# Optimization experiments

Hardware: AMD Instinct MI355X
Metric: run time of the kernel (lower is better)

Reference implementation:

```python
import jax, jax.numpy as jnp
import numpy as np

N = 20000
E = 320000
NEG_SLOPE = 0.2
BN_EPS = 1e-5


def _segment_softmax(e, dst, n):
    # e: [E, H] attention logits, dst: [E] destination node ids
    m = jax.ops.segment_max(e, dst, num_segments=n)           # [N, H]
    ex = jnp.exp(e - m[dst])                                   # [E, H]
    s = jax.ops.segment_sum(ex, dst, num_segments=n)          # [N, H]
    return ex / s[dst]


def gat_conv(x, src, dst, W, a_src, a_dst, b, heads, out_ch):
    # PyG GATConv (concat=True): h = x @ W reshaped to [N, H, C]
    n = x.shape[0]
    h = (x @ W).reshape(n, heads, out_ch)                      # [N, H, C]
    al_s = jnp.einsum('nhc,hc->nh', h, a_src)                  # [N, H]
    al_d = jnp.einsum('nhc,hc->nh', h, a_dst)
    e = jax.nn.leaky_relu(al_s[src] + al_d[dst], NEG_SLOPE)    # [E, H]
    alpha = _segment_softmax(e, dst, n)                        # [E, H]
    msg = h[src] * alpha[:, :, None]                           # [E, H, C]
    out = jax.ops.segment_sum(msg, dst, num_segments=n)        # [N, H, C]
    return out.reshape(n, heads * out_ch) + b


def batch_norm(x, gamma, beta):
    mu = jnp.mean(x, axis=0)
    var = jnp.mean((x - mu) ** 2, axis=0)  # biased, as torch BN training
    return gamma * (x - mu) * jax.lax.rsqrt(var + BN_EPS) + beta


def setup_inputs() -> dict:
    key = jax.random.key(0)
    ks = jax.random.split(key, 16)
    F_in, H1, C1 = 128, 8, 64
    D = H1 * C1  # 512
    OUT = 2
    def gl(k, shape, fan):
        return jax.random.normal(k, shape, dtype=jnp.float32) / np.sqrt(fan)
    x = jax.random.normal(ks[0], (N, F_in), dtype=jnp.float32)
    edge_index = jax.random.randint(ks[1], (2, E), 0, N, dtype=jnp.int64)
    return {
        'x': x, 'edge_index': edge_index,
        'W1': gl(ks[2], (F_in, H1 * C1), F_in),
        'a1s': gl(ks[3], (H1, C1), C1), 'a1d': gl(ks[4], (H1, C1), C1),
        'b1': jnp.zeros((D,), jnp.float32),
        'W2': gl(ks[5], (D, D), D),
        'a2s': gl(ks[6], (1, D), D), 'a2d': gl(ks[7], (1, D), D),
        'b2': jnp.zeros((D,), jnp.float32),
        'fc1_w': gl(ks[8], (D, D), D), 'fc1_b': jnp.zeros((D,), jnp.float32),
        'g1': jnp.ones((D,), jnp.float32), 'be1': jnp.zeros((D,), jnp.float32),
        'fc2_w': gl(ks[9], (D, D), D), 'fc2_b': jnp.zeros((D,), jnp.float32),
        'g2': jnp.ones((D,), jnp.float32), 'be2': jnp.zeros((D,), jnp.float32),
        'lin_w': gl(ks[10], (D, OUT), D), 'lin_b': jnp.zeros((OUT,), jnp.float32),
    }


def reference(x, edge_index, W1, a1s, a1d, b1, W2, a2s, a2d, b2,
              fc1_w, fc1_b, g1, be1, fc2_w, fc2_b, g2, be2, lin_w, lin_b):
    n = x.shape[0]
    loop = jnp.arange(n, dtype=edge_index.dtype)
    src = jnp.concatenate([edge_index[0], loop])  # add self-loops (PyG default)
    dst = jnp.concatenate([edge_index[1], loop])
    h = gat_conv(x, src, dst, W1, a1s, a1d, b1, heads=8, out_ch=64)
    h = batch_norm(jax.nn.relu(h @ fc1_w + fc1_b), g1, be1)
    h = gat_conv(h, src, dst, W2, a2s, a2d, b2, heads=1, out_ch=512)
    h = batch_norm(jax.nn.relu(h @ fc2_w + fc2_b), g2, be2)
    out = jax.nn.relu(h @ lin_w + lin_b)  # dropout p=0 is identity
    return out
```

## Files before the change

### kernel.cpp

```cpp
#include <hip/hip_runtime.h>
#include <hip/hip_bf16.h>

static constexpr int NN = 20000;
static constexpr int EE = 320000;
static constexpr int ET = EE + NN;
static constexpr int DD = 512;
static constexpr int FIN = 128;
static constexpr int ETP_MAX = ET + 7 * NN;

typedef __attribute__((ext_vector_type(8))) short short8;
typedef __attribute__((ext_vector_type(8))) unsigned short ushort8;
typedef __attribute__((ext_vector_type(4))) float f32x4;

__device__ __forceinline__ unsigned short f2bf(float f) {
    unsigned u = __float_as_uint(f);
    u += 0x7fffu + ((u >> 16) & 1u);
    return (unsigned short)(u >> 16);
}
__device__ __forceinline__ float bf2f(unsigned short b) {
    return __uint_as_float(((unsigned)b) << 16);
}

__device__ __forceinline__ void async_copy16(short* lds, const unsigned short* g) {
    __builtin_amdgcn_global_load_lds(
        (const __attribute__((address_space(1))) unsigned int*)g,
        (__attribute__((address_space(3))) unsigned int*)lds,
        16, 0, 0);
}

__global__ void scan_k(const int* __restrict__ deg, int* __restrict__ row_ptr,
                       int* __restrict__ perm) {
    __shared__ int part[1024];
    __shared__ int hist16[16][512];
    __shared__ int hbase[512];
    __shared__ int btot[512];
    int t = threadIdx.x;
    int wv = t >> 6;
    for (int k = t; k < 16 * 512; k += 1024) ((int*)hist16)[k] = 0;
    __syncthreads();
    const int CH = (NN + 1023) / 1024;
    int start = t * CH;
    int end = min(start + CH, NN);
    int dl[CH];
    int s = 0;
    for (int i = start; i < end; ++i) {
        int d = deg[i] + 1;
        dl[i - start] = d;
        s += (d + 7) & ~7;
        atomicAdd(&hist16[wv][min(d, 511)], 1);
    }
    part[t] = s;
    __syncthreads();
    if (t < 512) {
        int base = 0;
#pragma unroll
        for (int w = 0; w < 16; ++w) { int c = hist16[w][t]; hist16[w][t] = base; base += c; }
        btot[t] = base;
        hbase[t] = base;
    }
    __syncthreads();
    for (int off = 1; off < 512; off <<= 1) {
        int v = 0;
        if (t < 512 && t >= off) v = hbase[t - off];
        __syncthreads();
        if (t < 512) hbase[t] += v;
        __syncthreads();
    }
    if (t < 512) hbase[t] -= btot[t];
    for (int off = 1; off < 1024; off <<= 1) {
        int v = 0;
        if (t >= off) v = part[t - off];
        __syncthreads();
        part[t] += v;
        __syncthreads();
    }
    int base = (t == 0) ? 0 : part[t - 1];
    for (int i = start; i < end; ++i) { row_ptr[i] = base; base += (dl[i - start] + 7) & ~7; }
    if (t == 1023) row_ptr[NN] = part[1023];
    for (int i = start; i < end; ++i) {
        int d = min(dl[i - start], 511);
        int r = atomicAdd(&hist16[wv][d], 1);
        int pos = hbase[d] + r;
        perm[NN - 1 - pos] = i;
    }
}

static constexpr int TBLK = 208;
static constexpr int SZ_X4 = NN * FIN / 4;
static constexpr int XCB = (SZ_X4 + 255) / 256;
static constexpr int CDB = (EE + 255) / 256;
__global__ __launch_bounds__(256) void prep_all_k(
    const float* __restrict__ x, const float* __restrict__ W1,
    const float* __restrict__ fc1, const float* __restrict__ W2,
    const float* __restrict__ fc2,
    unsigned short* __restrict__ xb, unsigned short* __restrict__ W1t,
    unsigned short* __restrict__ fc1t, unsigned short* __restrict__ W2t,
    unsigned short* __restrict__ fc2t,
    const void* __restrict__ ei, int is64, int* __restrict__ deg) {
    int b = blockIdx.x;
    if (b < CDB) {
        int i = b * 256 + threadIdx.x;
        if (i < EE) {
            int d = is64 ? (int)((const long long*)ei)[EE + i] : ((const int*)ei)[EE + i];
            atomicAdd(&deg[d], 1);
        }
        return;
    }
    b -= CDB;
    if (b < TBLK) {
        __shared__ unsigned short tile[64][65];
        const float* src; unsigned short* dst; int rows, cols;
        if (b < 16)       { src = W1;  dst = W1t;  rows = FIN; cols = DD; }
        else if (b < 80)  { b -= 16;  src = fc1; dst = fc1t; rows = DD; cols = DD; }
        else if (b < 144) { b -= 80;  src = W2;  dst = W2t;  rows = DD; cols = DD; }
        else              { b -= 144; src = fc2; dst = fc2t; rows = DD; cols = DD; }
        int tc = cols / 64;
        int r0 = (b / tc) * 64, c0 = (b % tc) * 64;
        int t = threadIdx.x, lr = t >> 6, lc = t & 63;
#pragma unroll
        for (int p = 0; p < 16; ++p) {
            int r = lr + p * 4;
            tile[r][lc] = f2bf(src[(size_t)(r0 + r) * cols + c0 + lc]);
        }
        __syncthreads();
#pragma unroll
        for (int p = 0; p < 16; ++p) {
            int r = lr + p * 4;
            dst[(size_t)(c0 + r) * rows + r0 + lc] = tile[lc][r];
        }
        return;
    }
    int i = (b - TBLK) * 256 + threadIdx.x;
    if (i < SZ_X4) {
        float4 v = ((const float4*)x)[i];
        unsigned short o[4] = {f2bf(v.x), f2bf(v.y), f2bf(v.z), f2bf(v.w)};
        *(unsigned long long*)(xb + (size_t)i * 4) = *(const unsigned long long*)o;
    }
}

template <int RELU, int HASBIAS, int STATS, int ALS, int H, int FILLEX>
__global__ __launch_bounds__(256) void gemm_bf16(const unsigned short* __restrict__ A,
                                                 const unsigned short* __restrict__ Bt,
                                                 const float* __restrict__ bias,
                                                 unsigned short* __restrict__ Cb,
                                                 float* __restrict__ bnstat,
                                                 const float* __restrict__ avs,
                                                 const float* __restrict__ avd,
                                                 float* __restrict__ al_s,
                                                 float* __restrict__ al_d,
                                                 int M, int Nc, int K,
                                                 const void* __restrict__ ei, int is64,
                                                 const int* __restrict__ rp,
                                                 int* __restrict__ cursor,
                                                 int* __restrict__ csr_src,
                                                 int* __restrict__ csr_dst) {
    int id = blockIdx.x;
    if (FILLEX && id >= 640) {
        int e = (id - 640) * 256 + threadIdx.x;
        if (e >= ET) return;
        int s, d;
        if (e < EE) {
            if (is64) {
                const long long* p = (const long long*)ei;
                s = (int)p[e]; d = (int)p[EE + e];
            } else {
                const int* p = (const int*)ei;
                s = p[e]; d = p[EE + e];
            }
        } else {
            s = d = e - EE;
        }
        int pos = atomicAdd(&cursor[d], 1);
        int slot = rp[d] + pos;
        csr_src[slot] = s;
        csr_dst[slot] = d;
        return;
    }
    int bm = ((id >> 5) << 3) + (id & 7);
    int bn = (id >> 3) & 3;
    int m0 = bm * 128, n0 = bn * 128;
    if (m0 >= M) return;

    __shared__ short As0[128 * 32], As1[128 * 32];
    __shared__ short Bs0[128 * 32], Bs1[128 * 32];
    int t = threadIdx.x;
    int lane = t & 63, w = t >> 6;
    int wm = w & 1, wn = w >> 1;
    int quad = lane >> 4, mr = lane & 15;
    int lrow = lane >> 2;
    int lcol = (lane & 3) * 8;

    const unsigned short* Ag0 = A + (size_t)(m0 + w * 32 + lrow) * K + lcol;
    const unsigned short* Ag1 = A + (size_t)(m0 + w * 32 + 16 + lrow) * K + lcol;
    const unsigned short* Bg0 = Bt + (size_t)(n0 + w * 32 + lrow) * K + lcol;
    const unsigned short* Bg1 = Bt + (size_t)(n0 + w * 32 + 16 + lrow) * K + lcol;
    short* Al[2][2] = {{&As0[(w * 32) * 32], &As0[(w * 32 + 16) * 32]},
                       {&As1[(w * 32) * 32], &As1[(w * 32 + 16) * 32]}};
    short* Bl[2][2] = {{&Bs0[(w * 32) * 32], &Bs0[(w * 32 + 16) * 32]},
                       {&Bs1[(w * 32) * 32], &Bs1[(w * 32 + 16) * 32]}};

    f32x4 zero = {0.f, 0.f, 0.f, 0.f};
    f32x4 acc[4][4];
#pragma unroll
    for (int i = 0; i < 4; ++i)
#pragma unroll
        for (int j = 0; j < 4; ++j) acc[i][j] = zero;

    for (int k0 = 0; k0 < K; k0 += 64) {
        async_copy16(Al[0][0], Ag0 + k0);
        async_copy16(Al[1][0], Ag0 + k0 + 32);
        async_copy16(Al[0][1], Ag1 + k0);
        async_copy16(Al[1][1], Ag1 + k0 + 32);
        async_copy16(Bl[0][0], Bg0 + k0);
        async_copy16(Bl[1][0], Bg0 + k0 + 32);
        async_copy16(Bl[0][1], Bg1 + k0);
        async_copy16(Bl[1][1], Bg1 + k0 + 32);
        __syncthreads();
#pragma unroll
        for (int kp = 0; kp < 2; ++kp) {
            const short* Sa = kp ? As1 : As0;
            const short* Sb = kp ? Bs1 : Bs0;
            short8 af[4], bfr[4];
#pragma unroll
            for (int i = 0; i < 4; ++i) {
                af[i]  = *(const short8*)(&Sa[(wm * 64 + i * 16 + mr) * 32 + quad * 8]);
                bfr[i] = *(const short8*)(&Sb[(wn * 64 + i * 16 + mr) * 32 + quad * 8]);
            }
#pragma unroll
            for (int i = 0; i < 4; ++i)
#pragma unroll
                for (int j = 0; j < 4; ++j)
                    acc[i][j] = __builtin_amdgcn_mfma_f32_16x16x32_bf16(af[i], bfr[j], acc[i][j], 0, 0, 0);
        }
        __syncthreads();
    }

    float as_j[4], ad_j[4];
    if (ALS) {
#pragma unroll
        for (int j = 0; j < 4; ++j) {
            int n = n0 + wn * 64 + j * 16 + mr;
            as_j[j] = avs[n];
            ad_j[j] = avd[n];
        }
    }
    const int head = (H == 8) ? ((n0 + wn * 64) >> 6) : 0;
    float sj[4] = {0.f, 0.f, 0.f, 0.f}, qj[4] = {0.f, 0.f, 0.f, 0.f};
#pragma unroll
    for (int i = 0; i < 4; ++i) {
        int mb = m0 + wm * 64 + i * 16 + quad * 4;
#pragma unroll
        for (int r = 0; r < 4; ++r) {
            int m = mb + r;
            bool valid = (m < M);
            float ps = 0.f, pd = 0.f;
#pragma unroll
            for (int j = 0; j < 4; ++j) {
                int n = n0 + wn * 64 + j * 16 + mr;
                float v = acc[i][j][r];
                if (HASBIAS) v += bias[n];
                if (RELU) v = fmaxf(v, 0.f);
                unsigned short hb = f2bf(v);
                if (valid) Cb[(size_t)m * Nc + n] = hb;
                if (ALS) {
                    float vv = bf2f(hb);
                    ps += as_j[j] * vv;
                    pd += ad_j[j] * vv;
                }
                if (STATS && valid) { sj[j] += v; qj[j] += v * v; }
            }
            if (ALS) {
                ps += __shfl_xor(ps, 1); pd += __shfl_xor(pd, 1);
                ps += __shfl_xor(ps, 2); pd += __shfl_xor(pd, 2);
                ps += __shfl_xor(ps, 4); pd += __shfl_xor(pd, 4);
                ps += __shfl_xor(ps, 8); pd += __shfl_xor(pd, 8);
                if (mr == 0 && valid) {
                    if (H == 8) { al_s[m * 8 + head] = ps; al_d[m * 8 + head] = pd; }
                    else        { atomicAdd(&al_s[m], ps); atomicAdd(&al_d[m], pd); }
                }
            }
        }
    }
    if (STATS) {
#pragma unroll
        for (int j = 0; j < 4; ++j) {
            float s = sj[j], q = qj[j];
            s += __shfl_xor(s, 16); q += __shfl_xor(q, 16);
            s += __shfl_xor(s, 32); q += __shfl_xor(q, 32);
            if (lane < 16) {
                int n = n0 + wn * 64 + j * 16 + mr;
                atomicAdd(&bnstat[n], s);
                atomicAdd(&bnstat[512 + n], q);
            }
        }
    }
}

__global__ __launch_bounds__(256) void alpha1_k(const float* __restrict__ al_s,
                                                const float* __restrict__ al_d,
                                                const int* __restrict__ csr_src,
                                                const int* __restrict__ csr_dst,
                                                const int* __restrict__ row_ptr,
                                                unsigned short* __restrict__ es,
                                                float* __restrict__ al) {
    int p = blockIdx.x * blockDim.x + threadIdx.x;
    if (p >= row_ptr[NN]) return;
    int sn = csr_src[p];
    if (sn < 0) {
        es[p] = 0;
#pragma unroll
        for (int h = 0; h < 8; ++h) al[(size_t)h * ETP_MAX + p] = 0.f;
        return;
    }
    es[p] = (unsigned short)sn;
    int d = csr_dst[p];
    float4 s0 = *(const float4*)(al_s + (size_t)sn * 8);
    float4 s1 = *(const float4*)(al_s + (size_t)sn * 8 + 4);
    float4 d0 = *(const float4*)(al_d + (size_t)d * 8);
    float4 d1 = *(const float4*)(al_d + (size_t)d * 8 + 4);
    float l[8] = {s0.x + d0.x, s0.y + d0.y, s0.z + d0.z, s0.w + d0.w,
                  s1.x + d1.x, s1.y + d1.y, s1.z + d1.z, s1.w + d1.w};
#pragma unroll
    for (int h = 0; h < 8; ++h) {
        float xx = l[h];
        al[(size_t)h * ETP_MAX + p] = __expf((xx > 0.f) ? xx : 0.2f * xx);
    }
}

__global__ __launch_bounds__(256) void alpha2_k(const float* __restrict__ al_s,
                                                const float* __restrict__ al_d,
                                                const int* __restrict__ csr_src,
                                                const int* __restrict__ csr_dst,
                                                const int* __restrict__ row_ptr,
                                                float* __restrict__ al) {
    int p = blockIdx.x * blockDim.x + threadIdx.x;
    if (p >= row_ptr[NN]) return;
    int sn = csr_src[p];
    if (sn < 0) { al[p] = 0.f; return; }
    int d = csr_dst[p];
    float xx = al_s[sn] + al_d[d];
    al[p] = __expf((xx > 0.f) ? xx : 0.2f * xx);
}

template <int H>
__global__ __launch_bounds__(256) void gat_gather_k(const unsigned short* __restrict__ hb,
                                                    const unsigned short* __restrict__ es,
                                                    const float* __restrict__ alp,
                                                    const int* __restrict__ row_ptr,
                                                    const int* __restrict__ perm,
                                                    const float* __restrict__ bias,
                                                    unsigned short* __restrict__ outb) {
    int b = blockIdx.x;
    int s = b & 7;
    int g = b >> 3;
    int t = threadIdx.x;
    int w = t >> 6, lane = t & 63;
    int grp = lane >> 3, cg = lane & 7;
    int n = perm[g * 32 + w * 8 + grp];
    int col = s * 64 + cg * 8;
    const float* ap = alp + (H == 8 ? (size_t)s * ETP_MAX : (size_t)0);
    const char* hbase = (const char*)hb + col * 2;
    int beg = row_ptr[n];
    int nb = (row_ptr[n + 1] - beg) >> 3;

    float acc[8] = {0.f, 0.f, 0.f, 0.f, 0.f, 0.f, 0.f, 0.f};
    float psum = 0.f;
    ushort8 sv = *(const ushort8*)(es + beg);
    float4 a0 = *(const float4*)(ap + beg);
    float4 a1 = *(const float4*)(ap + beg + 4);
    for (int bb = 1; bb <= nb; ++bb) {
        short8 hreg[8];
#pragma unroll
        for (int u = 0; u < 8; ++u)
            hreg[u] = *(const short8*)(hbase + ((unsigned)sv[u] << 10));
        float av[8] = {a0.x, a0.y, a0.z, a0.w, a1.x, a1.y, a1.z, a1.w};
        ushort8 svn; float4 a0n, a1n;
        if (bb < nb) {
            int p0 = beg + bb * 8;
            svn = *(const ushort8*)(es + p0);
            a0n = *(const float4*)(ap + p0);
            a1n = *(const float4*)(ap + p0 + 4);
        }
#pragma unroll
        for (int u = 0; u < 8; ++u) psum += av[u];
#pragma unroll
        for (int u = 0; u < 8; ++u)
#pragma unroll
            for (int j = 0; j < 8; ++j)
                acc[j] = fmaf(av[u], bf2f((unsigned short)hreg[u][j]), acc[j]);
        if (bb < nb) { sv = svn; a0 = a0n; a1 = a1n; }
    }
    float inv = 1.0f / psum;
    unsigned short ov[8];
#pragma unroll
    for (int j = 0; j < 8; ++j) ov[j] = f2bf(acc[j] * inv + bias[col + j]);
    *(int4*)(outb + (size_t)n * DD + col) = *(const int4*)ov;
}

__global__ __launch_bounds__(256) void fold1_k(const float* __restrict__ stat,
                                               const float* __restrict__ g,
                                               const float* __restrict__ be,
                                               unsigned short* __restrict__ W2t,
                                               float* __restrict__ bias2) {
    int t = threadIdx.x;
    int n = blockIdx.x * 4 + (t >> 6);
    int lane = t & 63;
    float pb = 0.f;
#pragma unroll
    for (int j = 0; j < 8; ++j) {
        int k = lane * 8 + j;
        float mean = stat[k] * (1.0f / NN);
        float var = stat[512 + k] * (1.0f / NN) - mean * mean;
        float sc = g[k] * rsqrtf(var + 1e-5f);
        float sh = be[k] - mean * sc;
        float wv = bf2f(W2t[n * DD + k]);
        W2t[n * DD + k] = f2bf(sc * wv);
        pb += sh * wv;
    }
    for (int off = 32; off; off >>= 1) pb += __shfl_down(pb, off);
    if (lane == 0) bias2[n] = pb;
}

__global__ void bnfold2_k(const float* __restrict__ stat, const float* __restrict__ g,
                          const float* __restrict__ be, const float* __restrict__ lw,
                          const float* __restrict__ lb, float* __restrict__ w01,
                          float* __restrict__ kk) {
    __shared__ float r0[512], r1[512];
    int c = threadIdx.x;
    float mean = stat[c] * (1.0f / NN);
    float var = stat[512 + c] * (1.0f / NN) - mean * mean;
    float sc = g[c] * rsqrtf(var + 1e-5f);
    float sh = be[c] - mean * sc;
    float w0 = lw[2 * c], w1 = lw[2 * c + 1];
    w01[2 * c] = sc * w0;
    w01[2 * c + 1] = sc * w1;
    r0[c] = sh * w0;
    r1[c] = sh * w1;
    __syncthreads();
    for (int off = 256; off; off >>= 1) {
        if (c < off) { r0[c] += r0[c + off]; r1[c] += r1[c + off]; }
        __syncthreads();
    }
    if (c == 0) { kk[0] = r0[0] + lb[0]; kk[1] = r1[0] + lb[1]; }
}

__global__ void final_linear(const unsigned short* __restrict__ xb,
                             const float* __restrict__ w01, const float* __restrict__ kk,
                             float* __restrict__ out) {
    int wave = (blockIdx.x * blockDim.x + threadIdx.x) >> 6;
    int lane = threadIdx.x & 63;
    if (wave >= NN) return;
    short8 hv = *(const short8*)(xb + (size_t)wave * DD + lane * 8);
    float p0 = 0.f, p1 = 0.f;
#pragma unroll
    for (int j = 0; j < 8; ++j) {
        int c = lane * 8 + j;
        float h = bf2f((unsigned short)hv[j]);
        p0 = fmaf(h, w01[2 * c], p0);
        p1 = fmaf(h, w01[2 * c + 1], p1);
    }
    for (int off = 32; off; off >>= 1) {
        p0 += __shfl_down(p0, off);
        p1 += __shfl_down(p1, off);
    }
    if (lane == 0) {
        out[wave * 2 + 0] = fmaxf(p0 + kk[0], 0.f);
        out[wave * 2 + 1] = fmaxf(p1 + kk[1], 0.f);
    }
}

extern "C" void kernel_launch(void* const* d_in, const int* in_sizes, int n_in,
                              void* d_out, int out_size, void* d_ws, size_t ws_size,
                              hipStream_t stream) {
    const float* x     = (const float*)d_in[0];
    const void*  ei    = d_in[1];
    const float* W1    = (const float*)d_in[2];
    const float* a1s   = (const float*)d_in[3];
    const float* a1d   = (const float*)d_in[4];
    const float* b1    = (const float*)d_in[5];
    const float* W2    = (const float*)d_in[6];
    const float* a2s   = (const float*)d_in[7];
    const float* a2d   = (const float*)d_in[8];
    const float* b2    = (const float*)d_in[9];
    const float* fc1_w = (const float*)d_in[10];
    const float* fc1_b = (const float*)d_in[11];
    const float* g1    = (const float*)d_in[12];
    const float* be1   = (const float*)d_in[13];
    const float* fc2_w = (const float*)d_in[14];
    const float* fc2_b = (const float*)d_in[15];
    const float* g2    = (const float*)d_in[16];
    const float* be2   = (const float*)d_in[17];
    const float* lin_w = (const float*)d_in[18];
    const float* lin_b = (const float*)d_in[19];
    float* out = (float*)d_out;

    char* ws = (char*)d_ws;
    auto alloc = [&](size_t bytes) {
        void* p = (void*)ws;
        ws += (bytes + 255) & ~size_t(255);
        return p;
    };
    unsigned short* h_bf    = (unsigned short*)alloc((size_t)NN * DD * 2);
    unsigned short* act_bf  = (unsigned short*)alloc((size_t)NN * DD * 2);
    unsigned short* W1t     = (unsigned short*)alloc((size_t)DD * FIN * 2);
    unsigned short* fc1t    = (unsigned short*)alloc((size_t)DD * DD * 2);
    unsigned short* W2t     = (unsigned short*)alloc((size_t)DD * DD * 2);
    unsigned short* fc2t    = (unsigned short*)alloc((size_t)DD * DD * 2);
    float*          al_s    = (float*)alloc((size_t)NN * 8 * 4);
    float*          al_d    = (float*)alloc((size_t)NN * 8 * 4);
    int*            row_ptr = (int*)alloc((size_t)(NN + 1) * 4);
    int*            csr_dst = (int*)alloc((size_t)ETP_MAX * 4);
    int*            perm    = (int*)alloc((size_t)NN * 4);
    float*          bias2f  = (float*)alloc(512 * 4);
    float*          w01     = (float*)alloc(1024 * 4);
    float*          kkc     = (float*)alloc(256);
    unsigned short* ea_src  = (unsigned short*)alloc((size_t)ETP_MAX * 2);
    float*          ea_al   = (float*)alloc((size_t)8 * ETP_MAX * 4);
    int*            deg     = (int*)alloc((size_t)2 * NN * 4);
    int*            cursor  = deg + NN;
    float*          bnstatA = (float*)alloc((size_t)(2048 + 2 * NN) * 4);
    float*          bnstatB = bnstatA + 1024;
    float*          al_s2   = bnstatA + 2048;
    float*          al_d2   = al_s2 + NN;
    int*            csr_src = (int*)alloc((size_t)ETP_MAX * 4);

    const int is64 = (in_sizes[1] >= (int)(2u * EE * 8u)) ? 1 : 0;

    hipMemsetAsync(deg, 0, (size_t)2 * NN * 4, stream);
    hipMemsetAsync(bnstatA, 0, (size_t)(2048 + 2 * NN) * 4, stream);
    hipMemsetAsync(csr_src, 0xFF, (size_t)ETP_MAX * 4, stream);

    unsigned short* x_bf = act_bf;
    const int prep_blocks = CDB + TBLK + XCB;
    prep_all_k<<<prep_blocks, 256, 0, stream>>>(x, W1, fc1_w, W2, fc2_w,
                                                x_bf, W1t, fc1t, W2t, fc2t,
                                                ei, is64, deg);
    scan_k<<<1, 1024, 0, stream>>>(deg, row_ptr, perm);

    const int GB = 640;
    const int FB = (ET + 255) / 256;
    const int GGB = 8 * (NN / 32);
    const int AB = (ETP_MAX + 255) / 256;

    gemm_bf16<0, 0, 0, 1, 8, 1><<<GB + FB, 256, 0, stream>>>(
        x_bf, W1t, nullptr, h_bf, nullptr, a1s, a1d, al_s, al_d, NN, DD, FIN,
        ei, is64, row_ptr, cursor, csr_src, csr_dst);
    alpha1_k<<<AB, 256, 0, stream>>>(al_s, al_d, csr_src, csr_dst, row_ptr, ea_src, ea_al);
    gat_gather_k<8><<<GGB, 256, 0, stream>>>(h_bf, ea_src, ea_al, row_ptr, perm, b1, act_bf);
    gemm_bf16<1, 1, 1, 0, 8, 0><<<GB, 256, 0, stream>>>(
        act_bf, fc1t, fc1_b, h_bf, bnstatA, nullptr, nullptr, nullptr, nullptr, NN, DD, DD,
        nullptr, 0, nullptr, nullptr, nullptr, nullptr);
    fold1_k<<<128, 256, 0, stream>>>(bnstatA, g1, be1, W2t, bias2f);

    gemm_bf16<0, 1, 0, 1, 1, 0><<<GB, 256, 0, stream>>>(
        h_bf, W2t, bias2f, act_bf, nullptr, a2s, a2d, al_s2, al_d2, NN, DD, DD,
        nullptr, 0, nullptr, nullptr, nullptr, nullptr);
    alpha2_k<<<AB, 256, 0, stream>>>(al_s2, al_d2, csr_src, csr_dst, row_ptr, ea_al);
    gat_gather_k<1><<<GGB, 256, 0, stream>>>(act_bf, ea_src, ea_al, row_ptr, perm, b2, h_bf);
    gemm_bf16<1, 1, 1, 0, 8, 0><<<GB, 256, 0, stream>>>(
        h_bf, fc2t, fc2_b, act_bf, bnstatB, nullptr, nullptr, nullptr, nullptr, NN, DD, DD,
        nullptr, 0, nullptr, nullptr, nullptr, nullptr);

    bnfold2_k<<<1, 512, 0, stream>>>(bnstatB, g2, be2, lin_w, lin_b, w01, kkc);
    final_linear<<<(NN + 3) / 4, 256, 0, stream>>>(act_bf, w01, kkc, out);
}
```

Baseline: 336.3 us.

## Fuse layer-1 attention logits into gather, shrink CSR src to u16, fold BN2 into final

The separate alpha1 kernel is removed. The layer-1 gather now computes each edge's leaky-relu exp weight on the fly from the per-node al_s and al_d tables, so the 8-head edge-weight array is no longer written and read back. CSR source ids are stored as 16-bit values straight from the fill stage, which halves that buffer and drops the extra copy, with padding marked by 0xFFFF. The BN2 fold kernel is merged into final_linear, where every block recomputes the folded weights, and three memsets become two. The costs are redundant exp work per column slice in the gather and a per-block recomputation of the BN fold.

```diff
diff --git a/kernel.cpp b/kernel.cpp
--- a/kernel.cpp
+++ b/kernel.cpp
@@ -152,7 +152,7 @@
                                                  const void* __restrict__ ei, int is64,
                                                  const int* __restrict__ rp,
                                                  int* __restrict__ cursor,
-                                                 int* __restrict__ csr_src,
+                                                 unsigned short* __restrict__ csr_srcu,
                                                  int* __restrict__ csr_dst) {
     int id = blockIdx.x;
     if (FILLEX && id >= 640) {
@@ -172,7 +172,7 @@
         }
         int pos = atomicAdd(&cursor[d], 1);
         int slot = rp[d] + pos;
-        csr_src[slot] = s;
+        csr_srcu[slot] = (unsigned short)s;
         csr_dst[slot] = d;
         return;
     }
@@ -296,56 +296,26 @@
     }
 }
 
-__global__ __launch_bounds__(256) void alpha1_k(const float* __restrict__ al_s,
-                                                const float* __restrict__ al_d,
-                                                const int* __restrict__ csr_src,
-                                                const int* __restrict__ csr_dst,
-                                                const int* __restrict__ row_ptr,
-                                                unsigned short* __restrict__ es,
-                                                float* __restrict__ al) {
-    int p = blockIdx.x * blockDim.x + threadIdx.x;
-    if (p >= row_ptr[NN]) return;
-    int sn = csr_src[p];
-    if (sn < 0) {
-        es[p] = 0;
-#pragma unroll
-        for (int h = 0; h < 8; ++h) al[(size_t)h * ETP_MAX + p] = 0.f;
-        return;
-    }
-    es[p] = (unsigned short)sn;
-    int d = csr_dst[p];
-    float4 s0 = *(const float4*)(al_s + (size_t)sn * 8);
-    float4 s1 = *(const float4*)(al_s + (size_t)sn * 8 + 4);
-    float4 d0 = *(const float4*)(al_d + (size_t)d * 8);
-    float4 d1 = *(const float4*)(al_d + (size_t)d * 8 + 4);
-    float l[8] = {s0.x + d0.x, s0.y + d0.y, s0.z + d0.z, s0.w + d0.w,
-                  s1.x + d1.x, s1.y + d1.y, s1.z + d1.z, s1.w + d1.w};
-#pragma unroll
-    for (int h = 0; h < 8; ++h) {
-        float xx = l[h];
-        al[(size_t)h * ETP_MAX + p] = __expf((xx > 0.f) ? xx : 0.2f * xx);
-    }
-}
-
 __global__ __launch_bounds__(256) void alpha2_k(const float* __restrict__ al_s,
                                                 const float* __restrict__ al_d,
-                                                const int* __restrict__ csr_src,
+                                                const unsigned short* __restrict__ csr_srcu,
                                                 const int* __restrict__ csr_dst,
                                                 const int* __restrict__ row_ptr,
                                                 float* __restrict__ al) {
     int p = blockIdx.x * blockDim.x + threadIdx.x;
     if (p >= row_ptr[NN]) return;
-    int sn = csr_src[p];
-    if (sn < 0) { al[p] = 0.f; return; }
+    unsigned sn = csr_srcu[p];
+    if (sn == 0xFFFFu) { al[p] = 0.f; return; }
     int d = csr_dst[p];
     float xx = al_s[sn] + al_d[d];
-    al[p] = __expf((xx > 0.f) ? xx : 0.2f * xx);
+    al[p] = __expf(fmaxf(xx, 0.2f * xx));
 }
 
 template <int H>
 __global__ __launch_bounds__(256) void gat_gather_k(const unsigned short* __restrict__ hb,
-                                                    const unsigned short* __restrict__ es,
+                                                    const unsigned short* __restrict__ srcu,
                                                     const float* __restrict__ alp,
+                                                    const float* __restrict__ ald_t,
                                                     const int* __restrict__ row_ptr,
                                                     const int* __restrict__ perm,
                                                     const float* __restrict__ bias,
@@ -358,28 +328,51 @@
     int grp = lane >> 3, cg = lane & 7;
     int n = perm[g * 32 + w * 8 + grp];
     int col = s * 64 + cg * 8;
-    const float* ap = alp + (H == 8 ? (size_t)s * ETP_MAX : (size_t)0);
     const char* hbase = (const char*)hb + col * 2;
     int beg = row_ptr[n];
     int nb = (row_ptr[n + 1] - beg) >> 3;
+    const float* asp = alp + s;
+    float ald = (H == 8) ? ald_t[n * 8 + s] : 0.f;
 
     float acc[8] = {0.f, 0.f, 0.f, 0.f, 0.f, 0.f, 0.f, 0.f};
     float psum = 0.f;
-    ushort8 sv = *(const ushort8*)(es + beg);
-    float4 a0 = *(const float4*)(ap + beg);
-    float4 a1 = *(const float4*)(ap + beg + 4);
+    ushort8 sv = *(const ushort8*)(srcu + beg);
+    float4 a0, a1;
+    if (H == 1) { a0 = *(const float4*)(alp + beg); a1 = *(const float4*)(alp + beg + 4); }
     for (int bb = 1; bb <= nb; ++bb) {
+        unsigned sa[8];
+        float av[8];
+        if (H == 8) {
+#pragma unroll
+            for (int u = 0; u < 8; ++u) {
+                unsigned sn = sv[u];
+                bool pad = (sn == 0xFFFFu);
+                sa[u] = pad ? 0u : sn;
+                float xx = asp[(size_t)sa[u] * 8] + ald;
+                float a = __expf(fmaxf(xx, 0.2f * xx));
+                av[u] = pad ? 0.f : a;
+            }
+        } else {
+            float t8[8] = {a0.x, a0.y, a0.z, a0.w, a1.x, a1.y, a1.z, a1.w};
+#pragma unroll
+            for (int u = 0; u < 8; ++u) {
+                unsigned sn = sv[u];
+                sa[u] = (sn == 0xFFFFu) ? 0u : sn;
+                av[u] = t8[u];
+            }
+        }
         short8 hreg[8];
 #pragma unroll
         for (int u = 0; u < 8; ++u)
-            hreg[u] = *(const short8*)(hbase + ((unsigned)sv[u] << 10));
-        float av[8] = {a0.x, a0.y, a0.z, a0.w, a1.x, a1.y, a1.z, a1.w};
+            hreg[u] = *(const short8*)(hbase + ((size_t)sa[u] << 10));
         ushort8 svn; float4 a0n, a1n;
         if (bb < nb) {
             int p0 = beg + bb * 8;
-            svn = *(const ushort8*)(es + p0);
-            a0n = *(const float4*)(ap + p0);
-            a1n = *(const float4*)(ap + p0 + 4);
+            svn = *(const ushort8*)(srcu + p0);
+            if (H == 1) {
+                a0n = *(const float4*)(alp + p0);
+                a1n = *(const float4*)(alp + p0 + 4);
+            }
         }
 #pragma unroll
         for (int u = 0; u < 8; ++u) psum += av[u];
@@ -388,7 +381,7 @@
 #pragma unroll
             for (int j = 0; j < 8; ++j)
                 acc[j] = fmaf(av[u], bf2f((unsigned short)hreg[u][j]), acc[j]);
-        if (bb < nb) { sv = svn; a0 = a0n; a1 = a1n; }
+        if (bb < nb) { sv = svn; if (H == 1) { a0 = a0n; a1 = a1n; } }
     }
     float inv = 1.0f / psum;
     unsigned short ov[8];
@@ -421,35 +414,41 @@
     if (lane == 0) bias2[n] = pb;
 }
 
-__global__ void bnfold2_k(const float* __restrict__ stat, const float* __restrict__ g,
-                          const float* __restrict__ be, const float* __restrict__ lw,
-                          const float* __restrict__ lb, float* __restrict__ w01,
-                          float* __restrict__ kk) {
-    __shared__ float r0[512], r1[512];
-    int c = threadIdx.x;
-    float mean = stat[c] * (1.0f / NN);
-    float var = stat[512 + c] * (1.0f / NN) - mean * mean;
-    float sc = g[c] * rsqrtf(var + 1e-5f);
-    float sh = be[c] - mean * sc;
-    float w0 = lw[2 * c], w1 = lw[2 * c + 1];
-    w01[2 * c] = sc * w0;
-    w01[2 * c + 1] = sc * w1;
-    r0[c] = sh * w0;
-    r1[c] = sh * w1;
+__global__ __launch_bounds__(256) void final_linear(const unsigned short* __restrict__ xb,
+                                                    const float* __restrict__ stat,
+                                                    const float* __restrict__ g,
+                                                    const float* __restrict__ be,
+                                                    const float* __restrict__ lw,
+                                                    const float* __restrict__ lb,
+                                                    float* __restrict__ out) {
+    __shared__ float w01[1024];
+    __shared__ float red[512];
+    int t = threadIdx.x;
+    float rr0 = 0.f, rr1 = 0.f;
+#pragma unroll
+    for (int q = 0; q < 2; ++q) {
+        int c = t * 2 + q;
+        float mean = stat[c] * (1.0f / NN);
+        float var = stat[512 + c] * (1.0f / NN) - mean * mean;
+        float sc = g[c] * rsqrtf(var + 1e-5f);
+        float sh = be[c] - mean * sc;
+        float w0 = lw[2 * c], w1 = lw[2 * c + 1];
+        w01[2 * c] = sc * w0;
+        w01[2 * c + 1] = sc * w1;
+        rr0 = fmaf(sh, w0, rr0);
+        rr1 = fmaf(sh, w1, rr1);
+    }
+    red[t] = rr0;
+    red[256 + t] = rr1;
     __syncthreads();
-    for (int off = 256; off; off >>= 1) {
-        if (c < off) { r0[c] += r0[c + off]; r1[c] += r1[c + off]; }
-        __syncthreads();
-    }
-    if (c == 0) { kk[0] = r0[0] + lb[0]; kk[1] = r1[0] + lb[1]; }
-}
-
-__global__ void final_linear(const unsigned short* __restrict__ xb,
-                             const float* __restrict__ w01, const float* __restrict__ kk,
-                             float* __restrict__ out) {
-    int wave = (blockIdx.x * blockDim.x + threadIdx.x) >> 6;
-    int lane = threadIdx.x & 63;
-    if (wave >= NN) return;
+    for (int off = 128; off; off >>= 1) {
+        if (t < off) { red[t] += red[t + off]; red[256 + t] += red[256 + t + off]; }
+        __syncthreads();
+    }
+    float k0 = red[0] + lb[0], k1 = red[256] + lb[1];
+
+    int wave = blockIdx.x * 4 + (t >> 6);
+    int lane = t & 63;
     short8 hv = *(const short8*)(xb + (size_t)wave * DD + lane * 8);
     float p0 = 0.f, p1 = 0.f;
 #pragma unroll
@@ -464,8 +463,8 @@
         p1 += __shfl_down(p1, off);
     }
     if (lane == 0) {
-        out[wave * 2 + 0] = fmaxf(p0 + kk[0], 0.f);
-        out[wave * 2 + 1] = fmaxf(p1 + kk[1], 0.f);
+        out[wave * 2 + 0] = fmaxf(p0 + k0, 0.f);
+        out[wave * 2 + 1] = fmaxf(p1 + k1, 0.f);
     }
 }
 
@@ -512,23 +511,19 @@
     int*            csr_dst = (int*)alloc((size_t)ETP_MAX * 4);
     int*            perm    = (int*)alloc((size_t)NN * 4);
     float*          bias2f  = (float*)alloc(512 * 4);
-    float*          w01     = (float*)alloc(1024 * 4);
-    float*          kkc     = (float*)alloc(256);
-    unsigned short* ea_src  = (unsigned short*)alloc((size_t)ETP_MAX * 2);
-    float*          ea_al   = (float*)alloc((size_t)8 * ETP_MAX * 4);
-    int*            deg     = (int*)alloc((size_t)2 * NN * 4);
+    float*          ea_al   = (float*)alloc((size_t)ETP_MAX * 4);
+    int*            deg     = (int*)alloc((size_t)(4 * NN + 2048) * 4);
     int*            cursor  = deg + NN;
-    float*          bnstatA = (float*)alloc((size_t)(2048 + 2 * NN) * 4);
+    float*          bnstatA = (float*)(deg + 2 * NN);
     float*          bnstatB = bnstatA + 1024;
     float*          al_s2   = bnstatA + 2048;
     float*          al_d2   = al_s2 + NN;
-    int*            csr_src = (int*)alloc((size_t)ETP_MAX * 4);
+    unsigned short* csr_srcu = (unsigned short*)alloc((size_t)ETP_MAX * 2);
 
     const int is64 = (in_sizes[1] >= (int)(2u * EE * 8u)) ? 1 : 0;
 
-    hipMemsetAsync(deg, 0, (size_t)2 * NN * 4, stream);
-    hipMemsetAsync(bnstatA, 0, (size_t)(2048 + 2 * NN) * 4, stream);
-    hipMemsetAsync(csr_src, 0xFF, (size_t)ETP_MAX * 4, stream);
+    hipMemsetAsync(deg, 0, (size_t)(4 * NN + 2048) * 4, stream);
+    hipMemsetAsync(csr_srcu, 0xFF, (size_t)ETP_MAX * 2, stream);
 
     unsigned short* x_bf = act_bf;
     const int prep_blocks = CDB + TBLK + XCB;
@@ -544,9 +539,8 @@
 
     gemm_bf16<0, 0, 0, 1, 8, 1><<<GB + FB, 256, 0, stream>>>(
         x_bf, W1t, nullptr, h_bf, nullptr, a1s, a1d, al_s, al_d, NN, DD, FIN,
-        ei, is64, row_ptr, cursor, csr_src, csr_dst);
-    alpha1_k<<<AB, 256, 0, stream>>>(al_s, al_d, csr_src, csr_dst, row_ptr, ea_src, ea_al);
-    gat_gather_k<8><<<GGB, 256, 0, stream>>>(h_bf, ea_src, ea_al, row_ptr, perm, b1, act_bf);
+        ei, is64, row_ptr, cursor, csr_srcu, csr_dst);
+    gat_gather_k<8><<<GGB, 256, 0, stream>>>(h_bf, csr_srcu, al_s, al_d, row_ptr, perm, b1, act_bf);
     gemm_bf16<1, 1, 1, 0, 8, 0><<<GB, 256, 0, stream>>>(
         act_bf, fc1t, fc1_b, h_bf, bnstatA, nullptr, nullptr, nullptr, nullptr, NN, DD, DD,
         nullptr, 0, nullptr, nullptr, nullptr, nullptr);
@@ -555,12 +549,11 @@
     gemm_bf16<0, 1, 0, 1, 1, 0><<<GB, 256, 0, stream>>>(
         h_bf, W2t, bias2f, act_bf, nullptr, a2s, a2d, al_s2, al_d2, NN, DD, DD,
         nullptr, 0, nullptr, nullptr, nullptr, nullptr);
-    alpha2_k<<<AB, 256, 0, stream>>>(al_s2, al_d2, csr_src, csr_dst, row_ptr, ea_al);
-    gat_gather_k<1><<<GGB, 256, 0, stream>>>(act_bf, ea_src, ea_al, row_ptr, perm, b2, h_bf);
+    alpha2_k<<<AB, 256, 0, stream>>>(al_s2, al_d2, csr_srcu, csr_dst, row_ptr, ea_al);
+    gat_gather_k<1><<<GGB, 256, 0, stream>>>(act_bf, csr_srcu, ea_al, nullptr, row_ptr, perm, b2, h_bf);
     gemm_bf16<1, 1, 1, 0, 8, 0><<<GB, 256, 0, stream>>>(
         h_bf, fc2t, fc2_b, act_bf, bnstatB, nullptr, nullptr, nullptr, nullptr, NN, DD, DD,
         nullptr, 0, nullptr, nullptr, nullptr, nullptr);
 
-    bnfold2_k<<<1, 512, 0, stream>>>(bnstatB, g2, be2, lin_w, lin_b, w01, kkc);
-    final_linear<<<(NN + 3) / 4, 256, 0, stream>>>(act_bf, w01, kkc, out);
-}
+    final_linear<<<NN / 4, 256, 0, stream>>>(act_bf, bnstatB, g2, be2, lin_w, lin_b, out);
+}
```

After: 333.7 us. No clear change (-0.8%).
